# Kernel tuning notes

Measured on AMD Instinct MI355X. Metric: run time of the kernel, lower is better.

Reference implementation:

```python
import jax, jax.numpy as jnp
import numpy as np

BN_EPS = 1e-5


def setup_inputs() -> dict:
    key = jax.random.key(0)
    ks = jax.random.split(key, 11)
    B, C, Ci, D, H, W = 2, 256, 128, 8, 32, 32
    s = 0.02  # weight init scale
    return {
        "x": jax.random.normal(ks[0], (B, C, D, H, W), dtype=jnp.float32),
        "Wt": jax.random.normal(ks[1], (Ci, C), dtype=jnp.float32) * s,
        "bt": jax.random.normal(ks[2], (Ci,), dtype=jnp.float32) * s,
        "Wp": jax.random.normal(ks[3], (Ci, C), dtype=jnp.float32) * s,
        "bp": jax.random.normal(ks[4], (Ci,), dtype=jnp.float32) * s,
        "Wg": jax.random.normal(ks[5], (Ci, C), dtype=jnp.float32) * s,
        "bg": jax.random.normal(ks[6], (Ci,), dtype=jnp.float32) * s,
        "Ww": jax.random.normal(ks[7], (C, Ci), dtype=jnp.float32) * s,
        "bw": jax.random.normal(ks[8], (C,), dtype=jnp.float32) * s,
        "gamma": jax.random.normal(ks[9], (C,), dtype=jnp.float32),
        "beta": jax.random.normal(ks[10], (C,), dtype=jnp.float32),
    }


def reference(x, Wt, bt, Wp, bp, Wg, bg, Ww, bw, gamma, beta):
    # x: [B, C, D, H, W]; 1x1x1 Conv3d == per-position channel GEMM.
    B, C, D, H, W = x.shape
    xf = x.reshape(B, C, -1)  # [B, C, N], N = D*H*W

    theta = jnp.einsum('oc,bcn->bno', Wt, xf) + bt          # [B, N, Ci]
    phi = jnp.einsum('oc,bcn->bon', Wp, xf) + bp[None, :, None]  # [B, Ci, N]
    g = jnp.einsum('oc,bcn->bno', Wg, xf) + bg              # [B, N, Ci]

    # Unscaled, unmasked full self-attention over all N spatial positions.
    f = jnp.einsum('bnc,bcm->bnm', theta, phi)              # [B, N, N]
    a = jax.nn.softmax(f, axis=-1)
    y = jnp.einsum('bnm,bmc->bcn', a, g)                    # [B, Ci, N]

    # Output projection W: conv1x1 then BatchNorm3d (training-mode batch stats).
    wy = jnp.einsum('oc,bcn->bon', Ww, y) + bw[None, :, None]  # [B, C, N]
    mean = jnp.mean(wy, axis=(0, 2), keepdims=True)
    var = jnp.var(wy, axis=(0, 2), keepdims=True)
    wy_bn = (wy - mean) * jax.lax.rsqrt(var + BN_EPS)
    wy_bn = wy_bn * gamma[None, :, None] + beta[None, :, None]

    return wy_bn.reshape(B, C, D, H, W) + x
```

## Files before the change

### kernel.cpp

```cpp
#include <hip/hip_runtime.h>
#include <cstdint>
#include <cstddef>


typedef unsigned short u16;
typedef __bf16 bf16x8 __attribute__((ext_vector_type(8)));
typedef float f32x4 __attribute__((ext_vector_type(4)));
typedef float f32x16 __attribute__((ext_vector_type(16)));
typedef unsigned short u16x8 __attribute__((ext_vector_type(8)));

#define B_ 2
#define C_ 256
#define CI_ 128
#define N_ 8192
#define KVB 64

static __device__ __forceinline__ u16 f2bf(float f){
  unsigned u = __builtin_bit_cast(unsigned, f);
  unsigned r = (u + 0x7FFFu + ((u>>16)&1u)) >> 16;
  return (u16)r;
}
static __device__ __forceinline__ float bf2f(u16 v){
  unsigned u = ((unsigned)v) << 16;
  return __builtin_bit_cast(float, u);
}
static __device__ __forceinline__ float fexp2(float x){
  return __builtin_amdgcn_exp2f(x);
}
static __device__ __forceinline__ f32x4 f4zero(){
  f32x4 v; v[0]=0.f; v[1]=0.f; v[2]=0.f; v[3]=0.f; return v;
}
static __device__ __forceinline__ f32x16 f16zero(){
  f32x16 v;
#pragma unroll
  for (int i=0;i<16;i++) v[i]=0.f;
  return v;
}
static __device__ __forceinline__ f32x4 mfma16(bf16x8 a, bf16x8 b, f32x4 c){
  return __builtin_amdgcn_mfma_f32_16x16x32_bf16(a, b, c, 0, 0, 0);
}
static __device__ __forceinline__ f32x16 mfma32(bf16x8 a, bf16x8 b, f32x16 c){
  return __builtin_amdgcn_mfma_f32_32x32x16_bf16(a, b, c, 0, 0, 0);
}
static __device__ __forceinline__ unsigned cvtpk(float lo, float hi){
  unsigned r;
  asm("v_cvt_pk_bf16_f32 %0, %1, %2" : "=v"(r) : "v"(lo), "v"(hi));
  return r;
}
static __device__ __forceinline__ void plswap(unsigned &a, unsigned &b){
  asm volatile("v_permlane32_swap_b32 %0, %1" : "+v"(a), "+v"(b));
}

#define LOG2E 1.4426950408889634f

__global__ __launch_bounds__(256) void k1_proj(const float* __restrict__ x,
     const float* __restrict__ Wt, const float* __restrict__ Wp,
     const float* __restrict__ Wg, const float* __restrict__ bt,
     const float* __restrict__ bp, const float* __restrict__ bg,
     u16* __restrict__ theta, u16* __restrict__ kproj, u16* __restrict__ gT,
     float* __restrict__ stats){
  __shared__ u16 At[64*264];
  __shared__ u16 Wt_[32*264];
  __shared__ u16 gbuf[32*72];
  int tid = threadIdx.x;
  int b  = blockIdx.x >> 7;
  int nb = (blockIdx.x & 127) * 64;
  int w = tid >> 6, lane = tid & 63;
  int l15 = lane & 15, kg = lane >> 4;

  if (blockIdx.x == 0){
    stats[tid] = 0.f; stats[256 + tid] = 0.f;
  }

  {
    int cp = tid & 127, nh = tid >> 7;
    int c0 = cp*2;
    const float* src0 = x + ((size_t)(b*C_ + c0))*N_ + nb + nh*32;
    const float* src1 = src0 + N_;
#pragma unroll
    for (int j=0;j<8;j++){
      f32x4 a = *(const f32x4*)(src0 + j*4);
      f32x4 c = *(const f32x4*)(src1 + j*4);
#pragma unroll
      for (int q=0;q<4;q++){
        unsigned pk = (unsigned)f2bf(a[q]) | ((unsigned)f2bf(c[q])<<16);
        *(unsigned*)&At[(nh*32 + j*4 + q)*264 + c0] = pk;
      }
    }
  }
  __syncthreads();

  bf16x8 afr[8];
#pragma unroll
  for (int kc=0;kc<8;kc++)
    afr[kc] = *(const bf16x8*)&At[(w*16+l15)*264 + kc*32 + kg*8];

  for (int och = 0; och < 12; och++){
    {
      int o8 = tid>>3, cp8 = tid&7;
      const float* wsel = (och<4) ? (Wt + ((size_t)(och*32 + o8))*256)
                        : (och<8) ? (Wp + ((size_t)((och-4)*32 + o8))*256)
                                  : (Wg + ((size_t)((och-8)*32 + o8))*256);
      float scl = (och<4) ? LOG2E : 1.f;
#pragma unroll
      for (int j=0;j<4;j++){
        f32x4 w0 = *(const f32x4*)(wsel + cp8*8 + j*64);
        f32x4 w1 = *(const f32x4*)(wsel + cp8*8 + j*64 + 4);
        u16 tmp[8];
#pragma unroll
        for (int q=0;q<4;q++){ tmp[q] = f2bf(w0[q]*scl); tmp[4+q] = f2bf(w1[q]*scl); }
        *(u16x8*)&Wt_[o8*264 + cp8*8 + j*64] = *(const u16x8*)tmp;
      }
    }
    __syncthreads();

    f32x4 acc0 = f4zero(), acc1 = f4zero();
#pragma unroll
    for (int kc=0;kc<8;kc++){
      bf16x8 b0 = *(const bf16x8*)&Wt_[(l15)*264 + kc*32 + kg*8];
      bf16x8 b1 = *(const bf16x8*)&Wt_[(16+l15)*264 + kc*32 + kg*8];
      acc0 = mfma16(afr[kc], b0, acc0);
      acc1 = mfma16(afr[kc], b1, acc1);
    }

    if (och < 8){
      u16* dst = (och < 4) ? theta : kproj;
      int oo = (och & 3) * 32;
#pragma unroll
      for (int of=0;of<2;of++){
        int o = oo + of*16 + l15;
        float bias = (och<4) ? bt[och*32 + of*16 + l15] * LOG2E
                             : bp[(och-4)*32 + of*16 + l15];
        f32x4 acc = of ? acc1 : acc0;
#pragma unroll
        for (int i=0;i<4;i++){
          int n = nb + w*16 + kg*4 + i;
          dst[((size_t)b*N_ + n)*CI_ + o] = f2bf(acc[i] + bias);
        }
      }
      __syncthreads();
    } else {
#pragma unroll
      for (int of=0;of<2;of++){
        int o = of*16 + l15;
        float bias = bg[(och-8)*32 + of*16 + l15];
        f32x4 acc = of ? acc1 : acc0;
#pragma unroll
        for (int i=0;i<4;i++){
          int r = w*16 + kg*4 + i;
          gbuf[o*72 + r] = f2bf(acc[i] + bias);
        }
      }
      __syncthreads();
      {
        int o = tid>>3, np = tid&7;
        int og = (och-8)*32 + o;
        u16x8 v = *(const u16x8*)&gbuf[o*72 + np*8];
        *(u16x8*)(gT + ((size_t)b*CI_ + og)*N_ + nb + np*8) = v;
      }
      __syncthreads();
    }
  }
}

__global__ __launch_bounds__(512, 2) void k2_attn(const u16* __restrict__ theta,
      const u16* __restrict__ kproj, const u16* __restrict__ gT,
      u16* __restrict__ pO, float* __restrict__ pM, float* __restrict__ pL){
  constexpr int CHUNK_N = 2048;
  constexpr int NTI = CHUNK_N / KVB;
  constexpr int NS  = NTI/2;
  __shared__ char smem[131072];
  char* kbase = smem;
  char* vbase = smem + 65536;
  int tid = threadIdx.x;
  int bid = blockIdx.x;
  int combo = bid & 7;
  int b = combo & 1;
  int chunk = combo >> 1;
  int qblk = bid >> 3;
  int n0 = chunk * CHUNK_N;
  int w = tid >> 6, lane = tid & 63;
  int l31 = lane & 31, hi = lane >> 5;
  int qg = qblk*256 + w*32 + l31;

  bf16x8 qf[8];
  {
    const u16* qsrc = theta + ((size_t)b*N_ + qg)*CI_ + hi*8;
#pragma unroll
    for (int cc=0; cc<8; cc++) qf[cc] = *(const bf16x8*)(qsrc + cc*16);
  }

  int krow_s = tid >> 3, kpart = tid & 7;
  int vrow_s = tid >> 2, vpart = tid & 3;
  const u16* ksrc = kproj + ((size_t)b*N_ + n0 + krow_s)*CI_ + kpart*16;
  const u16* vsrc = gT + ((size_t)b*CI_ + vrow_s)*N_ + n0 + vpart*16;
  int kw_off[2], vw_off[2];
#pragma unroll
  for (int j=0;j<2;j++){
    int cb = kpart*32 + j*16;
    kw_off[j] = krow_s*256 + (cb ^ ((krow_s&15)<<4));
    int kb = vpart*32 + j*16;
    vw_off[j] = vrow_s*128 + (kb ^ ((vrow_s&7)<<4));
  }
  int kswz = (l31&15)<<4;
  int vswz = (l31&7)<<4;
  int kro[8], vro[4];
#pragma unroll
  for (int cc=0;cc<8;cc++) kro[cc] = l31*256 + ((cc*32 + hi*16) ^ kswz);
#pragma unroll
  for (int ks=0;ks<4;ks++) vro[ks] = l31*128 + ((ks*32 + hi*16) ^ vswz);

#pragma unroll
  for (int j=0;j<2;j++){
    *(u16x8*)(kbase + kw_off[j])         = *(const u16x8*)(ksrc + j*8);
    *(u16x8*)(kbase + 16384 + kw_off[j]) = *(const u16x8*)(ksrc + (size_t)KVB*CI_ + j*8);
    *(u16x8*)(vbase + vw_off[j])         = *(const u16x8*)(vsrc + j*8);
    *(u16x8*)(vbase + 16384 + vw_off[j]) = *(const u16x8*)(vsrc + KVB + j*8);
  }
  __syncthreads();

  f32x16 oacc[4];
#pragma unroll
  for (int i=0;i<4;i++) oacc[i] = f16zero();
  float mrun = -1e30f, lrun = 0.f;

#define K2_TILE(KB, VB) { \
    f32x16 sA = f16zero(), sB = f16zero(); \
    __builtin_amdgcn_s_setprio(1); \
    _Pragma("unroll") \
    for (int cc=0; cc<8; cc++){ \
      bf16x8 kf0 = *(const bf16x8*)((KB) + kro[cc]); \
      bf16x8 kf1 = *(const bf16x8*)((KB) + 8192 + kro[cc]); \
      sA = mfma32(kf0, qf[cc], sA); \
      sB = mfma32(kf1, qf[cc], sB); \
    } \
    __builtin_amdgcn_s_setprio(0); \
    float t8[8]; \
    _Pragma("unroll") \
    for (int i=0;i<8;i++) t8[i] = fmaxf(fmaxf(sA[i], sA[i+8]), fmaxf(sB[i], sB[i+8])); \
    float mx = fmaxf(fmaxf(fmaxf(t8[0],t8[4]),fmaxf(t8[1],t8[5])), \
                     fmaxf(fmaxf(t8[2],t8[6]),fmaxf(t8[3],t8[7]))); \
    mx = fmaxf(mx, __shfl_xor(mx, 32)); \
    if (__any(mx > mrun + 12.f)){ \
      float mnew = fmaxf(mrun, mx); \
      float sc = fexp2(mrun - mnew); \
      lrun *= sc; \
      _Pragma("unroll") \
      for (int i=0;i<4;i++){ _Pragma("unroll") for (int r=0;r<16;r++) oacc[i][r] *= sc; } \
      mrun = mnew; } \
    float pA[16], pB[16]; \
    _Pragma("unroll") \
    for (int r=0;r<16;r++){ pA[r] = fexp2(sA[r]-mrun); pB[r] = fexp2(sB[r]-mrun); } \
    { float s8[8]; \
      _Pragma("unroll") \
      for (int i=0;i<8;i++) s8[i] = (pA[i]+pA[i+8]) + (pB[i]+pB[i+8]); \
      float ps = ((s8[0]+s8[4])+(s8[1]+s8[5])) + ((s8[2]+s8[6])+(s8[3]+s8[7])); \
      ps += __shfl_xor(ps, 32); lrun += ps; } \
    __builtin_amdgcn_s_setprio(1); \
    _Pragma("unroll") \
    for (int ks=0; ks<4; ks++){ \
      const float* P = (ks<2) ? pA : pB; \
      int r0 = (ks&1)*8; \
      unsigned a0 = cvtpk(P[r0+0], P[r0+1]); \
      unsigned b0 = cvtpk(P[r0+4], P[r0+5]); \
      unsigned a1 = cvtpk(P[r0+2], P[r0+3]); \
      unsigned b1 = cvtpk(P[r0+6], P[r0+7]); \
      plswap(a0, b0); plswap(a1, b1); \
      union { unsigned u[4]; bf16x8 v; } pb; \
      pb.u[0]=a0; pb.u[1]=a1; pb.u[2]=b0; pb.u[3]=b1; \
      _Pragma("unroll") \
      for (int c2=0; c2<4; c2++){ \
        bf16x8 vf = *(const bf16x8*)((VB) + c2*4096 + vro[ks]); \
        oacc[c2] = mfma32(vf, pb.v, oacc[c2]); \
      } \
    } \
    __builtin_amdgcn_s_setprio(0); }

  for (int s = 0; s < NS; s++){
    int H = s & 1;
    char* kh = kbase + H*32768;
    char* vh = vbase + H*32768;
    u16x8 kst[4], vst[4];
    bool pf = (s+1 < NS);
    if (pf){
      const u16* ks = ksrc + (size_t)(2*s+2)*KVB*CI_;
      const u16* vs = vsrc + (2*s+2)*KVB;
      kst[0] = *(const u16x8*)(ks);
      kst[1] = *(const u16x8*)(ks + 8);
      kst[2] = *(const u16x8*)(ks + (size_t)KVB*CI_);
      kst[3] = *(const u16x8*)(ks + (size_t)KVB*CI_ + 8);
      vst[0] = *(const u16x8*)(vs);
      vst[1] = *(const u16x8*)(vs + 8);
      vst[2] = *(const u16x8*)(vs + KVB);
      vst[3] = *(const u16x8*)(vs + KVB + 8);
    }

    K2_TILE(kh, vh)

    if (pf){
      char* kd = kbase + (H^1)*32768;
      char* vd = vbase + (H^1)*32768;
#pragma unroll
      for (int j=0;j<2;j++){
        *(u16x8*)(kd + kw_off[j])         = kst[j];
        *(u16x8*)(kd + 16384 + kw_off[j]) = kst[2+j];
        *(u16x8*)(vd + vw_off[j])         = vst[j];
        *(u16x8*)(vd + 16384 + vw_off[j]) = vst[2+j];
      }
    }

    K2_TILE(kh + 16384, vh + 16384)

    __syncthreads();
  }

  char* region = smem + w*8192;
#pragma unroll
  for (int c2=0;c2<4;c2++)
#pragma unroll
    for (int r=0;r<16;r++){
      int c = c2*32 + (r&3) + 8*(r>>2) + 4*hi;
      *(u16*)(region + l31*256 + ((c*2) ^ vswz)) = f2bf(oacc[c2][r]);
    }
  __syncthreads();
  {
    int ql = lane >> 1, half = lane & 1;
    int qg2 = qblk*256 + w*32 + ql;
    u16* dst = pO + ((size_t)(chunk*2 + b)*N_ + qg2)*CI_ + half*64;
    int rswz = (ql&7)<<4;
#pragma unroll
    for (int j=0;j<8;j++){
      u16x8 v2 = *(const u16x8*)(region + ql*256 + ((half*128 + j*16) ^ rswz));
      *(u16x8*)(dst + j*8) = v2;
    }
  }
  if (hi == 0){
    pM[(size_t)(chunk*2 + b)*N_ + qg] = mrun;
    pL[(size_t)(chunk*2 + b)*N_ + qg] = lrun;
  }
}

__global__ __launch_bounds__(256) void k3_wy(const u16* __restrict__ pO,
    const float* __restrict__ pM, const float* __restrict__ pL,
    const float* __restrict__ Ww, const float* __restrict__ bw,
    u16* __restrict__ wy, float* __restrict__ stats){
  __shared__ u16 Yt[64*136];
  __shared__ u16 Wt_[64*136];
  __shared__ float wyb[64*72];
  int tid = threadIdx.x;
  int b  = blockIdx.x >> 7;
  int nb = (blockIdx.x & 127) * 64;
  int w = tid>>6, lane = tid&63;
  int l15 = lane&15, kg = lane>>4;

  {
    int n = tid>>2, cp = tid&3;
    size_t q = (size_t)nb + n;
    float m[4], l[4];
#pragma unroll
    for (int ch=0; ch<4; ch++){
      m[ch] = pM[(size_t)(ch*2+b)*N_ + q];
      l[ch] = pL[(size_t)(ch*2+b)*N_ + q];
    }
    float M = fmaxf(fmaxf(m[0],m[1]), fmaxf(m[2],m[3]));
    float wts[4]; float L = 0.f;
#pragma unroll
    for (int ch=0; ch<4; ch++){ wts[ch] = exp2f(m[ch]-M); L += wts[ch]*l[ch]; }
    float inv = 1.f/L;
#pragma unroll
    for (int j=0;j<4;j++){
      int c0 = cp*32 + j*8;
      float acc[8];
#pragma unroll
      for (int i=0;i<8;i++) acc[i]=0.f;
#pragma unroll
      for (int ch=0; ch<4; ch++){
        u16x8 v = *(const u16x8*)(pO + ((size_t)(ch*2+b)*N_ + q)*CI_ + c0);
#pragma unroll
        for (int i=0;i<8;i++) acc[i] += wts[ch]*bf2f(v[i]);
      }
#pragma unroll
      for (int i=0;i<4;i++){
        unsigned pk = (unsigned)f2bf(acc[2*i]*inv) | ((unsigned)f2bf(acc[2*i+1]*inv)<<16);
        *(unsigned*)&Yt[n*136 + c0 + 2*i] = pk;
      }
    }
  }
  __syncthreads();

  bf16x8 afr[4];
#pragma unroll
  for (int kc=0;kc<4;kc++)
    afr[kc] = *(const bf16x8*)&Yt[(w*16+l15)*136 + kc*32 + kg*8];

  for (int oc=0; oc<4; oc++){
    {
      int o = tid>>2, cp = tid&3;
      const float* src = Ww + ((size_t)(oc*64 + o))*CI_ + cp*32;
#pragma unroll
      for (int j=0;j<4;j++){
        f32x4 w0 = *(const f32x4*)(src + j*8);
        f32x4 w1 = *(const f32x4*)(src + j*8 + 4);
        u16 tmp[8];
#pragma unroll
        for (int q2=0;q2<4;q2++){ tmp[q2] = f2bf(w0[q2]); tmp[4+q2] = f2bf(w1[q2]); }
        *(u16x8*)&Wt_[o*136 + cp*32 + j*8] = *(const u16x8*)tmp;
      }
    }
    __syncthreads();

    f32x4 acc[4];
#pragma unroll
    for (int of=0;of<4;of++) acc[of] = f4zero();
#pragma unroll
    for (int kc=0;kc<4;kc++){
#pragma unroll
      for (int of=0;of<4;of++){
        bf16x8 bfr = *(const bf16x8*)&Wt_[(of*16+l15)*136 + kc*32 + kg*8];
        acc[of] = mfma16(afr[kc], bfr, acc[of]);
      }
    }
#pragma unroll
    for (int of=0;of<4;of++){
#pragma unroll
      for (int i=0;i<4;i++)
        wyb[(of*16+l15)*72 + w*16 + kg*4 + i] = acc[of][i];
    }
    __syncthreads();
    {
      int o = tid>>2, np = tid&3;
      int og = oc*64 + o;
      float bias = bw[og];
      float sm = 0.f, sq = 0.f;
      u16* dst = wy + ((size_t)b*C_ + og)*N_ + nb + np*16;
      u16 buf[16];
#pragma unroll
      for (int j=0;j<4;j++){
#pragma unroll
        for (int q2=0;q2<4;q2++){
          float t2 = wyb[o*72 + np*16 + j*4 + q2] + bias;
          buf[j*4+q2] = f2bf(t2); sm += t2; sq += t2*t2;
        }
      }
      *(u16x8*)dst = *(const u16x8*)&buf[0];
      *(u16x8*)(dst+8) = *(const u16x8*)&buf[8];
      sm += __shfl_xor(sm, 1); sm += __shfl_xor(sm, 2);
      sq += __shfl_xor(sq, 1); sq += __shfl_xor(sq, 2);
      if ((tid&3)==0){
        atomicAdd(&stats[og], sm);
        atomicAdd(&stats[256+og], sq);
      }
    }
    __syncthreads();
  }
}

__global__ __launch_bounds__(256) void k4_bn(const u16* __restrict__ wy,
    const float* __restrict__ x, const float* __restrict__ stats,
    const float* __restrict__ gamma, const float* __restrict__ beta,
    float* __restrict__ out){
  size_t base = ((size_t)blockIdx.x)*2048 + (size_t)threadIdx.x*8;
  int o = (int)((base >> 13) & 255);
  const float invn = 1.f/16384.f;
  float mean = stats[o]*invn;
  float var  = stats[256+o]*invn - mean*mean;
  float rs = rsqrtf(var + 1e-5f);
  float g = gamma[o]*rs;
  float bb = beta[o];
  u16x8 a = *(const u16x8*)(wy + base);
  f32x4 x0 = *(const f32x4*)(x + base);
  f32x4 x1 = *(const f32x4*)(x + base + 4);
  f32x4 r0, r1;
#pragma unroll
  for (int q=0;q<4;q++){
    r0[q] = (bf2f(a[q])-mean)*g + bb + x0[q];
    r1[q] = (bf2f(a[4+q])-mean)*g + bb + x1[q];
  }
  *(f32x4*)(out + base)     = r0;
  *(f32x4*)(out + base + 4) = r1;
}

extern "C" void kernel_launch(void* const* d_in, const int* in_sizes, int n_in,
                              void* d_out, int out_size, void* d_ws, size_t ws_size,
                              hipStream_t stream){
  const float* x     = (const float*)d_in[0];
  const float* Wt    = (const float*)d_in[1];
  const float* bt    = (const float*)d_in[2];
  const float* Wp    = (const float*)d_in[3];
  const float* bp    = (const float*)d_in[4];
  const float* Wg    = (const float*)d_in[5];
  const float* bg    = (const float*)d_in[6];
  const float* Ww    = (const float*)d_in[7];
  const float* bw    = (const float*)d_in[8];
  const float* gamma = (const float*)d_in[9];
  const float* beta  = (const float*)d_in[10];

  char* ws = (char*)d_ws;
  u16*   theta = (u16*)(ws + 0);
  u16*   kproj = (u16*)(ws + 4194304);
  u16*   gT    = (u16*)(ws + 8388608);
  u16*   pO    = (u16*)(ws + 12582912);
  float* pM    = (float*)(ws + 29360128);
  float* pL    = (float*)(ws + 29622272);
  u16*   wy    = (u16*)(ws + 29884416);
  float* stats = (float*)(ws + 38273024);
  float* out   = (float*)d_out;

  k1_proj<<<256, 256, 0, stream>>>(x, Wt, Wp, Wg, bt, bp, bg, theta, kproj, gT, stats);
  k2_attn<<<256, 512, 0, stream>>>(theta, kproj, gT, pO, pM, pL);
  k3_wy<<<256, 256, 0, stream>>>(pO, pM, pL, Ww, bw, wy, stats);
  k4_bn<<<2048, 256, 0, stream>>>(wy, x, stats, gamma, beta, out);
}
```

Before: 132.6 us.

## Double block size in projection and output kernels, splitting output channels across halves

k1_proj and k3_wy now launch 512 threads per block. The two 256-thread halves each process half of the output-channel chunks using separate shared-memory weight buffers, which doubles in-block parallelism for these small grids of 256 blocks. k1 also writes gT directly with packed 8-byte stores instead of staging through shared memory, which removes two barriers per chunk. k3 uses fexp2 for the merge weights. The cost is more shared memory per block and narrower, less coalesced gT stores.

```diff
diff --git a/kernel.cpp b/kernel.cpp
--- a/kernel.cpp
+++ b/kernel.cpp
@@ -53,38 +53,37 @@
 
 #define LOG2E 1.4426950408889634f
 
-__global__ __launch_bounds__(256) void k1_proj(const float* __restrict__ x,
+__global__ __launch_bounds__(512) void k1_proj(const float* __restrict__ x,
      const float* __restrict__ Wt, const float* __restrict__ Wp,
      const float* __restrict__ Wg, const float* __restrict__ bt,
      const float* __restrict__ bp, const float* __restrict__ bg,
      u16* __restrict__ theta, u16* __restrict__ kproj, u16* __restrict__ gT,
      float* __restrict__ stats){
   __shared__ u16 At[64*264];
-  __shared__ u16 Wt_[32*264];
-  __shared__ u16 gbuf[32*72];
+  __shared__ u16 Wt2[2][32*264];
   int tid = threadIdx.x;
   int b  = blockIdx.x >> 7;
   int nb = (blockIdx.x & 127) * 64;
   int w = tid >> 6, lane = tid & 63;
   int l15 = lane & 15, kg = lane >> 4;
-
-  if (blockIdx.x == 0){
-    stats[tid] = 0.f; stats[256 + tid] = 0.f;
-  }
+  int half = w >> 2, wq = w & 3;
+  int ht = tid & 255;
+
+  if (blockIdx.x == 0){ stats[tid] = 0.f; }
 
   {
     int cp = tid & 127, nh = tid >> 7;
     int c0 = cp*2;
-    const float* src0 = x + ((size_t)(b*C_ + c0))*N_ + nb + nh*32;
+    const float* src0 = x + ((size_t)(b*C_ + c0))*N_ + nb + nh*16;
     const float* src1 = src0 + N_;
 #pragma unroll
-    for (int j=0;j<8;j++){
+    for (int j=0;j<4;j++){
       f32x4 a = *(const f32x4*)(src0 + j*4);
       f32x4 c = *(const f32x4*)(src1 + j*4);
 #pragma unroll
       for (int q=0;q<4;q++){
         unsigned pk = (unsigned)f2bf(a[q]) | ((unsigned)f2bf(c[q])<<16);
-        *(unsigned*)&At[(nh*32 + j*4 + q)*264 + c0] = pk;
+        *(unsigned*)&At[(nh*16 + j*4 + q)*264 + c0] = pk;
       }
     }
   }
@@ -93,11 +92,12 @@
   bf16x8 afr[8];
 #pragma unroll
   for (int kc=0;kc<8;kc++)
-    afr[kc] = *(const bf16x8*)&At[(w*16+l15)*264 + kc*32 + kg*8];
-
-  for (int och = 0; och < 12; och++){
+    afr[kc] = *(const bf16x8*)&At[(wq*16+l15)*264 + kc*32 + kg*8];
+
+  for (int i = 0; i < 6; i++){
+    int och = half*6 + i;
     {
-      int o8 = tid>>3, cp8 = tid&7;
+      int o8 = ht>>3, cp8 = ht&7;
       const float* wsel = (och<4) ? (Wt + ((size_t)(och*32 + o8))*256)
                         : (och<8) ? (Wp + ((size_t)((och-4)*32 + o8))*256)
                                   : (Wg + ((size_t)((och-8)*32 + o8))*256);
@@ -109,7 +109,7 @@
         u16 tmp[8];
 #pragma unroll
         for (int q=0;q<4;q++){ tmp[q] = f2bf(w0[q]*scl); tmp[4+q] = f2bf(w1[q]*scl); }
-        *(u16x8*)&Wt_[o8*264 + cp8*8 + j*64] = *(const u16x8*)tmp;
+        *(u16x8*)&Wt2[half][o8*264 + cp8*8 + j*64] = *(const u16x8*)tmp;
       }
     }
     __syncthreads();
@@ -117,8 +117,8 @@
     f32x4 acc0 = f4zero(), acc1 = f4zero();
 #pragma unroll
     for (int kc=0;kc<8;kc++){
-      bf16x8 b0 = *(const bf16x8*)&Wt_[(l15)*264 + kc*32 + kg*8];
-      bf16x8 b1 = *(const bf16x8*)&Wt_[(16+l15)*264 + kc*32 + kg*8];
+      bf16x8 b0 = *(const bf16x8*)&Wt2[half][(l15)*264 + kc*32 + kg*8];
+      bf16x8 b1 = *(const bf16x8*)&Wt2[half][(16+l15)*264 + kc*32 + kg*8];
       acc0 = mfma16(afr[kc], b0, acc0);
       acc1 = mfma16(afr[kc], b1, acc1);
     }
@@ -133,33 +133,25 @@
                              : bp[(och-4)*32 + of*16 + l15];
         f32x4 acc = of ? acc1 : acc0;
 #pragma unroll
-        for (int i=0;i<4;i++){
-          int n = nb + w*16 + kg*4 + i;
-          dst[((size_t)b*N_ + n)*CI_ + o] = f2bf(acc[i] + bias);
+        for (int i2=0;i2<4;i2++){
+          int n = nb + wq*16 + kg*4 + i2;
+          dst[((size_t)b*N_ + n)*CI_ + o] = f2bf(acc[i2] + bias);
         }
       }
-      __syncthreads();
     } else {
 #pragma unroll
       for (int of=0;of<2;of++){
         int o = of*16 + l15;
-        float bias = bg[(och-8)*32 + of*16 + l15];
+        int og = (och-8)*32 + o;
+        float bias = bg[og];
         f32x4 acc = of ? acc1 : acc0;
-#pragma unroll
-        for (int i=0;i<4;i++){
-          int r = w*16 + kg*4 + i;
-          gbuf[o*72 + r] = f2bf(acc[i] + bias);
-        }
-      }
-      __syncthreads();
-      {
-        int o = tid>>3, np = tid&7;
-        int og = (och-8)*32 + o;
-        u16x8 v = *(const u16x8*)&gbuf[o*72 + np*8];
-        *(u16x8*)(gT + ((size_t)b*CI_ + og)*N_ + nb + np*8) = v;
-      }
-      __syncthreads();
-    }
+        unsigned lo = (unsigned)f2bf(acc[0]+bias) | ((unsigned)f2bf(acc[1]+bias)<<16);
+        unsigned hi2 = (unsigned)f2bf(acc[2]+bias) | ((unsigned)f2bf(acc[3]+bias)<<16);
+        uint2 val; val.x = lo; val.y = hi2;
+        *(uint2*)(gT + ((size_t)b*CI_ + og)*N_ + nb + wq*16 + kg*4) = val;
+      }
+    }
+    __syncthreads();
   }
 }
 
@@ -340,21 +332,23 @@
   }
 }
 
-__global__ __launch_bounds__(256) void k3_wy(const u16* __restrict__ pO,
+__global__ __launch_bounds__(512) void k3_wy(const u16* __restrict__ pO,
     const float* __restrict__ pM, const float* __restrict__ pL,
     const float* __restrict__ Ww, const float* __restrict__ bw,
     u16* __restrict__ wy, float* __restrict__ stats){
   __shared__ u16 Yt[64*136];
-  __shared__ u16 Wt_[64*136];
-  __shared__ float wyb[64*72];
+  __shared__ u16 Wt2[2][64*136];
+  __shared__ float wyb2[2][64*72];
   int tid = threadIdx.x;
   int b  = blockIdx.x >> 7;
   int nb = (blockIdx.x & 127) * 64;
   int w = tid>>6, lane = tid&63;
   int l15 = lane&15, kg = lane>>4;
+  int half = w >> 2, wq = w & 3;
+  int ht = tid & 255;
 
   {
-    int n = tid>>2, cp = tid&3;
+    int n = tid>>3, cp = tid&7;
     size_t q = (size_t)nb + n;
     float m[4], l[4];
 #pragma unroll
@@ -365,11 +359,11 @@
     float M = fmaxf(fmaxf(m[0],m[1]), fmaxf(m[2],m[3]));
     float wts[4]; float L = 0.f;
 #pragma unroll
-    for (int ch=0; ch<4; ch++){ wts[ch] = exp2f(m[ch]-M); L += wts[ch]*l[ch]; }
+    for (int ch=0; ch<4; ch++){ wts[ch] = fexp2(m[ch]-M); L += wts[ch]*l[ch]; }
     float inv = 1.f/L;
 #pragma unroll
-    for (int j=0;j<4;j++){
-      int c0 = cp*32 + j*8;
+    for (int j=0;j<2;j++){
+      int c0 = cp*16 + j*8;
       float acc[8];
 #pragma unroll
       for (int i=0;i<8;i++) acc[i]=0.f;
@@ -391,12 +385,13 @@
   bf16x8 afr[4];
 #pragma unroll
   for (int kc=0;kc<4;kc++)
-    afr[kc] = *(const bf16x8*)&Yt[(w*16+l15)*136 + kc*32 + kg*8];
-
-  for (int oc=0; oc<4; oc++){
+    afr[kc] = *(const bf16x8*)&Yt[(wq*16+l15)*136 + kc*32 + kg*8];
+
+  for (int i = 0; i < 2; i++){
+    int oc = half*2 + i;
     {
-      int o = tid>>2, cp = tid&3;
-      const float* src = Ww + ((size_t)(oc*64 + o))*CI_ + cp*32;
+      int o = ht>>2, cp4 = ht&3;
+      const float* src = Ww + ((size_t)(oc*64 + o))*CI_ + cp4*32;
 #pragma unroll
       for (int j=0;j<4;j++){
         f32x4 w0 = *(const f32x4*)(src + j*8);
@@ -404,7 +399,7 @@
         u16 tmp[8];
 #pragma unroll
         for (int q2=0;q2<4;q2++){ tmp[q2] = f2bf(w0[q2]); tmp[4+q2] = f2bf(w1[q2]); }
-        *(u16x8*)&Wt_[o*136 + cp*32 + j*8] = *(const u16x8*)tmp;
+        *(u16x8*)&Wt2[half][o*136 + cp4*32 + j*8] = *(const u16x8*)tmp;
       }
     }
     __syncthreads();
@@ -416,19 +411,19 @@
     for (int kc=0;kc<4;kc++){
 #pragma unroll
       for (int of=0;of<4;of++){
-        bf16x8 bfr = *(const bf16x8*)&Wt_[(of*16+l15)*136 + kc*32 + kg*8];
+        bf16x8 bfr = *(const bf16x8*)&Wt2[half][(of*16+l15)*136 + kc*32 + kg*8];
         acc[of] = mfma16(afr[kc], bfr, acc[of]);
       }
     }
 #pragma unroll
     for (int of=0;of<4;of++){
 #pragma unroll
-      for (int i=0;i<4;i++)
-        wyb[(of*16+l15)*72 + w*16 + kg*4 + i] = acc[of][i];
+      for (int i2=0;i2<4;i2++)
+        wyb2[half][(of*16+l15)*72 + wq*16 + kg*4 + i2] = acc[of][i2];
     }
     __syncthreads();
     {
-      int o = tid>>2, np = tid&3;
+      int o = ht>>2, np = ht&3;
       int og = oc*64 + o;
       float bias = bw[og];
       float sm = 0.f, sq = 0.f;
@@ -438,7 +433,7 @@
       for (int j=0;j<4;j++){
 #pragma unroll
         for (int q2=0;q2<4;q2++){
-          float t2 = wyb[o*72 + np*16 + j*4 + q2] + bias;
+          float t2 = wyb2[half][o*72 + np*16 + j*4 + q2] + bias;
           buf[j*4+q2] = f2bf(t2); sm += t2; sq += t2*t2;
         }
       }
@@ -506,8 +501,8 @@
   float* stats = (float*)(ws + 38273024);
   float* out   = (float*)d_out;
 
-  k1_proj<<<256, 256, 0, stream>>>(x, Wt, Wp, Wg, bt, bp, bg, theta, kproj, gT, stats);
+  k1_proj<<<256, 512, 0, stream>>>(x, Wt, Wp, Wg, bt, bp, bg, theta, kproj, gT, stats);
   k2_attn<<<256, 512, 0, stream>>>(theta, kproj, gT, pO, pM, pL);
-  k3_wy<<<256, 256, 0, stream>>>(pO, pM, pL, Ww, bw, wy, stats);
+  k3_wy<<<256, 512, 0, stream>>>(pO, pM, pL, Ww, bw, wy, stats);
   k4_bn<<<2048, 256, 0, stream>>>(wy, x, stats, gamma, beta, out);
 }
```

After: 125.1 us. 1.06x faster.
